# Kernel optimization log

Hardware: AMD Instinct MI355X
Metric: run time of the kernel (lower is better)

The kernel has to match this reference:

```python
import math
import jax, jax.numpy as jnp
import numpy as np
from jax import lax

# ---- static config (mirrors RPN init + typical torchvision anchor setup) ----
IMG_H = IMG_W = 800
LEVELS = [(200, 200, 4, 32), (100, 100, 8, 64), (50, 50, 16, 128), (25, 25, 32, 256), (13, 13, 64, 512)]  # (h, w, stride, anchor_size)
RATIOS = (0.5, 1.0, 2.0)
COUNTS = tuple(h * w * len(RATIOS) for (h, w, _, _) in LEVELS)  # (120000,30000,7500,1875,507)
A_TOTAL = sum(COUNTS)  # 159882
PRE_NMS = 2000
POST_NMS = 1000
NMS_THRESH = 0.7
MIN_SIZE = 1e-3
BBOX_CLIP = math.log(1000.0 / 16)


def make_anchors():
    parts = []
    for (h, w, stride, size) in LEVELS:
        ws = np.array([size * np.sqrt(1.0 / r) for r in RATIOS], np.float32)  # [3]
        hs = np.array([size * np.sqrt(r) for r in RATIOS], np.float32)
        sx = (np.arange(w, dtype=np.float32) + 0.5) * stride
        sy = (np.arange(h, dtype=np.float32) + 0.5) * stride
        cy, cx = np.meshgrid(sy, sx, indexing='ij')
        cx = cx.reshape(-1, 1)
        cy = cy.reshape(-1, 1)
        a = np.stack([cx - ws / 2, cy - hs / 2, cx + ws / 2, cy + hs / 2], axis=-1)  # [HW,3,4]
        parts.append(a.reshape(-1, 4))
    return np.concatenate(parts, 0).astype(np.float32)


def setup_inputs() -> dict:
    key = jax.random.key(0)
    k1, k2 = jax.random.split(key)
    scores = jax.random.normal(k1, (1, A_TOTAL), dtype=jnp.float32)
    deltas = jax.random.normal(k2, (A_TOTAL, 4), dtype=jnp.float32) * 0.5
    anchors = jnp.asarray(make_anchors())
    return {'scores': scores, 'deltas': deltas, 'anchors': anchors}


def _pairwise_iou(b):
    area = (b[:, 2] - b[:, 0]) * (b[:, 3] - b[:, 1])  # [K]
    lt = jnp.maximum(b[:, None, :2], b[None, :, :2])   # [K,K,2]
    rb = jnp.minimum(b[:, None, 2:], b[None, :, 2:])
    wh = jnp.maximum(rb - lt, 0.0)
    inter = wh[..., 0] * wh[..., 1]
    return inter / (area[:, None] + area[None, :] - inter)


def reference(scores, deltas, anchors):
    s_all = lax.stop_gradient(scores[0])  # original does cls.detach()
    # ---- box decode (torchvision-style) ----
    w = anchors[:, 2] - anchors[:, 0]
    h = anchors[:, 3] - anchors[:, 1]
    cx = anchors[:, 0] + 0.5 * w
    cy = anchors[:, 1] + 0.5 * h
    dx, dy = deltas[:, 0], deltas[:, 1]
    dw = jnp.minimum(deltas[:, 2], BBOX_CLIP)
    dh = jnp.minimum(deltas[:, 3], BBOX_CLIP)
    px = cx + dx * w
    py = cy + dy * h
    pw = jnp.exp(dw) * w
    ph = jnp.exp(dh) * h
    boxes = jnp.stack([px - 0.5 * pw, py - 0.5 * ph, px + 0.5 * pw, py + 0.5 * ph], axis=1)  # [A,4]
    # ---- per-level top-k over objectness ----
    idx_parts = []
    off = 0
    for c in COUNTS:
        k = min(PRE_NMS, c)
        _, ti = lax.top_k(lax.dynamic_slice_in_dim(s_all, off, c), k)
        idx_parts.append(ti + off)
        off += c
    top_idx = jnp.concatenate(idx_parts)  # [K=8382]
    K = top_idx.shape[0]
    s = s_all[top_idx]
    b = boxes[top_idx]
    # ---- clip to image + min-size validity (masked instead of compacted) ----
    b = jnp.stack([jnp.clip(b[:, 0], 0.0, IMG_W), jnp.clip(b[:, 1], 0.0, IMG_H),
                   jnp.clip(b[:, 2], 0.0, IMG_W), jnp.clip(b[:, 3], 0.0, IMG_H)], axis=1)
    valid = ((b[:, 2] - b[:, 0]) >= MIN_SIZE) & ((b[:, 3] - b[:, 1]) >= MIN_SIZE)
    # ---- per-level NMS offset; replicates original feature_mask[keep] indexing
    # (positional indexing into the full anchor-order level-id vector) ----
    fmask_full = np.concatenate([np.full(c, i, np.float32) for i, c in enumerate(COUNTS)])
    fmask = jnp.asarray(fmask_full[:K])
    box_max = jnp.max(jnp.where(valid[:, None], b, -jnp.inf))
    bn = b + (fmask * (box_max + 1.0))[:, None]
    # ---- greedy NMS on score-sorted candidates ----
    s_m = jnp.where(valid, s, -jnp.inf)
    order = jnp.argsort(-s_m)
    s_srt = s_m[order]
    b_srt = b[order]
    iou = _pairwise_iou(bn[order])  # [K,K] ~281MB
    ar = jnp.arange(K)

    def body(i, keep):
        sup = (iou[i] > NMS_THRESH) & (ar > i)
        return jnp.where(keep[i], keep & ~sup, keep)

    keep = lax.fori_loop(0, K, body, s_srt > -jnp.inf)
    final = jnp.where(keep, s_srt, -jnp.inf)
    out_s, oidx = lax.top_k(final, POST_NMS)  # top post_nms kept, score order; -inf pads
    out_b = b_srt[oidx]
    return out_b, out_s
```

## Files before the change

kernel.cpp:

```cpp
#include <hip/hip_runtime.h>
#include <math.h>

typedef unsigned int u32;
typedef unsigned long long u64;
typedef unsigned char u8;

#define K_TOT 8382
#define NCH 131
#define SC 4
#define NSC ((NCH + SC - 1) / SC)
#define CAP 1024
#define GCAP 32768
#define IMGSZ 800.0f

__device__ __constant__ int LOFF[5] = {0, 120000, 150000, 157500, 159375};
__device__ __constant__ int LCNT[5] = {120000, 30000, 7500, 1875, 507};
__device__ __constant__ int KSEL[5] = {2000, 2000, 2000, 1875, 507};
__device__ __constant__ int SELB[5] = {0, 2000, 4000, 6000, 7875};
__device__ __constant__ int HBS[4] = {0, 118, 148, 156};
__device__ __constant__ int GBS[6] = {0, 118, 148, 156, 158, 159};

static __device__ __forceinline__ u32 fkey(float x) {
    u32 u = __float_as_uint(x);
    u32 m = (u32)(((int)u) >> 31) | 0x80000000u;
    return u ^ m;
}

static __device__ __forceinline__ int lvl_of(int s) {
    return (s < 2000) ? 0 : (s < 4000) ? 1 : (s < 6000) ? 2 : (s < 7875) ? 3 : 4;
}

static __device__ __forceinline__ u32 rdl32(u32 v, int j) {
    return (u32)__builtin_amdgcn_readlane((int)v, j);
}
static __device__ __forceinline__ u64 rdlane64(u64 v, int j) {
    u32 lo = (u32)__builtin_amdgcn_readlane((int)(u32)v, j);
    u32 hi = (u32)__builtin_amdgcn_readlane((int)(u32)(v >> 32), j);
    return ((u64)hi << 32) | (u64)lo;
}

static __device__ __forceinline__ u32 wor32(u32 x) {
    x |= (u32)__builtin_amdgcn_update_dpp(0, (int)x, 0x111, 0xf, 0xf, true);
    x |= (u32)__builtin_amdgcn_update_dpp(0, (int)x, 0x112, 0xf, 0xf, true);
    x |= (u32)__builtin_amdgcn_update_dpp(0, (int)x, 0x114, 0xf, 0xf, true);
    x |= (u32)__builtin_amdgcn_update_dpp(0, (int)x, 0x118, 0xf, 0xf, true);
    x |= (u32)__builtin_amdgcn_update_dpp(0, (int)x, 0x142, 0xa, 0xf, true);
    x |= (u32)__builtin_amdgcn_update_dpp(0, (int)x, 0x143, 0xc, 0xf, true);
    return x;
}

static __device__ __forceinline__ void thresh_scan(const u32* hist, u32* scanbuf, int m,
                                                   u32 need, u32* sv, int t) {
    for (int i = t; i < m; i += 1024) scanbuf[i] = hist[m - 1 - i];
    __syncthreads();
    for (int ofs = 1; ofs < m; ofs <<= 1) {
        int i0 = t, i1 = t + 1024;
        u32 a0 = 0, a1 = 0;
        if (i0 < m && i0 >= ofs) a0 = scanbuf[i0 - ofs];
        if (i1 < m && i1 >= ofs) a1 = scanbuf[i1 - ofs];
        __syncthreads();
        if (i0 < m && i0 >= ofs) scanbuf[i0] += a0;
        if (i1 < m && i1 >= ofs) scanbuf[i1] += a1;
        __syncthreads();
    }
    for (int i = t; i < m; i += 1024) {
        u32 inc = scanbuf[i];
        u32 exc = i ? scanbuf[i - 1] : 0;
        if (inc >= need && exc < need) { sv[0] = (u32)(m - 1 - i); sv[1] = need - exc; }
    }
    __syncthreads();
}

__global__ __launch_bounds__(1024) void k_hist(const float* __restrict__ scores,
                                               u32* __restrict__ hist3) {
    __shared__ u32 lh[2048];
    int t = threadIdx.x;
    lh[t] = 0; lh[t + 1024] = 0;
    __syncthreads();
    int b = blockIdx.x;
    int l = (b < HBS[1]) ? 0 : (b < HBS[2]) ? 1 : 2;
    int i = (b - HBS[l]) * 1024 + t;
    if (i < LCNT[l]) atomicAdd(&lh[fkey(scores[LOFF[l] + i]) >> 21], 1u);
    __syncthreads();
    u32* h = hist3 + l * 2048;
    if (lh[t]) atomicAdd(&h[t], lh[t]);
    if (lh[t + 1024]) atomicAdd(&h[t + 1024], lh[t + 1024]);
}

__global__ __launch_bounds__(1024) void k_thresh(const u32* __restrict__ hist3,
                                                 u32* __restrict__ tinfo) {
    __shared__ u32 scanbuf[2048];
    __shared__ u32 sv[2];
    int l = blockIdx.x;
    int t = threadIdx.x;
    thresh_scan(hist3 + l * 2048, scanbuf, 2048, (u32)KSEL[l], sv, t);
    if (t == 0) { tinfo[l * 2] = sv[0]; tinfo[l * 2 + 1] = sv[1]; }
}

__global__ __launch_bounds__(1024) void k_gather(const float* __restrict__ scores,
                                                 const u32* __restrict__ tinfo,
                                                 u32* __restrict__ sel, u32* __restrict__ cgt,
                                                 u32* __restrict__ gcnt, u32* __restrict__ gidx,
                                                 u32* __restrict__ gkey) {
    int b = blockIdx.x;
    int l = (b < GBS[1]) ? 0 : (b < GBS[2]) ? 1 : (b < GBS[3]) ? 2 : (b < GBS[4]) ? 3 : 4;
    int i = (b - GBS[l]) * 1024 + threadIdx.x;
    if (i >= LCNT[l]) return;
    int off = LOFF[l], sb = SELB[l];
    if (l >= 3) { sel[sb + i] = (u32)(off + i); return; }
    u32 ky = fkey(scores[off + i]);
    u32 b1 = tinfo[l * 2];
    u32 top = ky >> 21;
    if (top > b1) {
        u32 p = atomicAdd(&cgt[l], 1u);
        sel[sb + p] = (u32)(off + i);
    } else if (top == b1) {
        u32 e = atomicAdd(&gcnt[l], 1u);
        if (e < GCAP) { gidx[l * GCAP + e] = (u32)i; gkey[l * GCAP + e] = ky; }
    }
}

__global__ __launch_bounds__(1024) void k_final(const u32* __restrict__ gidx,
                                                const u32* __restrict__ gkey,
                                                const u32* __restrict__ gcnt,
                                                const u32* __restrict__ tinfo,
                                                u32* __restrict__ sel) {
    __shared__ u32 hist[2048];
    __shared__ u32 scanbuf[2048];
    __shared__ u32 eqbuf[1024];
    __shared__ u32 sv[2];
    __shared__ u32 c2, ceq;
    int l = blockIdx.x;
    int t = threadIdx.x;
    int k = KSEL[l], sb = SELB[l], off = LOFF[l];
    u32 m = gcnt[l]; if (m > GCAP) m = GCAP;
    u32 b1 = tinfo[l * 2];
    u32 need = tinfo[l * 2 + 1];
    const u32* kb = gkey + l * GCAP;
    const u32* ib = gidx + l * GCAP;
    hist[t] = 0; hist[t + 1024] = 0; __syncthreads();
    for (u32 e = t; e < m; e += 1024) atomicAdd(&hist[(kb[e] >> 10) & 2047u], 1u);
    __syncthreads();
    thresh_scan(hist, scanbuf, 2048, need, sv, t);
    u32 b2 = sv[0], need2 = sv[1];
    __syncthreads();
    hist[t] = 0; __syncthreads();
    for (u32 e = t; e < m; e += 1024) {
        u32 ky = kb[e];
        if (((ky >> 10) & 2047u) == b2) atomicAdd(&hist[ky & 1023u], 1u);
    }
    __syncthreads();
    thresh_scan(hist, scanbuf, 1024, need2, sv, t);
    u32 T = (b1 << 21) | (b2 << 10) | sv[0];
    u32 take = sv[1];
    if (t == 0) { c2 = 0; ceq = 0; }
    __syncthreads();
    u32 nGTbin = need - take;
    u32 base2 = (u32)sb + (u32)k - need;
    for (u32 e = t; e < m; e += 1024) {
        u32 ky = kb[e];
        if (ky > T) { u32 p = atomicAdd(&c2, 1u); sel[base2 + p] = (u32)off + ib[e]; }
        else if (ky == T) { u32 q = atomicAdd(&ceq, 1u); if (q < 1024) eqbuf[q] = ib[e]; }
    }
    __syncthreads();
    if (t == 0) {
        int n = (ceq > 1024u) ? 1024 : (int)ceq;
        for (int a = 1; a < n; ++a) {
            u32 v = eqbuf[a]; int bq = a - 1;
            while (bq >= 0 && eqbuf[bq] > v) { eqbuf[bq + 1] = eqbuf[bq]; --bq; }
            eqbuf[bq + 1] = v;
        }
        for (u32 q = 0; q < take; ++q) sel[base2 + nGTbin + q] = (u32)off + eqbuf[q];
    }
}

__global__ void k_decode(const float* __restrict__ scores, const float4* __restrict__ deltas,
                         const float4* __restrict__ anchors, const u32* __restrict__ sel,
                         float4* __restrict__ candB, float* __restrict__ candS,
                         u32* __restrict__ candV, u32* __restrict__ candA) {
    int s = blockIdx.x * 256 + threadIdx.x;
    if (s >= K_TOT) return;
    u32 a = sel[s];
    float4 an = anchors[a];
    float4 dl = deltas[a];
    float sc = scores[a];
    float w = __fsub_rn(an.z, an.x), h = __fsub_rn(an.w, an.y);
    float cx = __fadd_rn(an.x, __fmul_rn(0.5f, w));
    float cy = __fadd_rn(an.y, __fmul_rn(0.5f, h));
    const float CLIPV = (float)4.1351665567423563;
    float dw = fminf(dl.z, CLIPV);
    float dh = fminf(dl.w, CLIPV);
    float px = __fadd_rn(cx, __fmul_rn(dl.x, w));
    float py = __fadd_rn(cy, __fmul_rn(dl.y, h));
    float pw = __fmul_rn((float)exp((double)dw), w);
    float ph = __fmul_rn((float)exp((double)dh), h);
    float x1 = __fsub_rn(px, __fmul_rn(0.5f, pw));
    float y1 = __fsub_rn(py, __fmul_rn(0.5f, ph));
    float x2 = __fadd_rn(px, __fmul_rn(0.5f, pw));
    float y2 = __fadd_rn(py, __fmul_rn(0.5f, ph));
    x1 = fminf(fmaxf(x1, 0.0f), IMGSZ);
    y1 = fminf(fmaxf(y1, 0.0f), IMGSZ);
    x2 = fminf(fmaxf(x2, 0.0f), IMGSZ);
    y2 = fminf(fmaxf(y2, 0.0f), IMGSZ);
    bool valid = (__fsub_rn(x2, x1) >= 0.001f) && (__fsub_rn(y2, y1) >= 0.001f);
    candB[s] = make_float4(x1, y1, x2, y2);
    candS[s] = sc;
    candV[s] = valid ? 1u : 0u;
    candA[s] = a;
}

__global__ __launch_bounds__(256) void k_rank_lvl(const float* __restrict__ candS,
                                                  const u32* __restrict__ candA,
                                                  u32* __restrict__ Praw) {
    __shared__ u64 tile[256];
    int l = blockIdx.z;
    int cnt = KSEL[l], base = SELB[l];
    int tx = blockIdx.x * 256;
    int ty = blockIdx.y * 256;
    if (tx >= cnt || ty >= cnt) return;
    int t = threadIdx.x;
    u64 Aj = ~0ull;
    if (tx + t < cnt) {
        int j = base + tx + t;
        Aj = ((u64)(~fkey(candS[j])) << 32) | (u64)candA[j];
    }
    tile[t] = Aj;
    __syncthreads();
    int si = ty + t;
    if (si >= cnt) return;
    int s = base + si;
    u64 A = ((u64)(~fkey(candS[s])) << 32) | (u64)candA[s];
    int r = 0;
#pragma unroll 8
    for (int q = 0; q < 256; ++q) r += (tile[q] < A);
    if (r) atomicAdd(&Praw[s], (u32)r);
}

__global__ __launch_bounds__(256) void k_rank_glob(const float* __restrict__ candS,
                                                   const u32* __restrict__ candV,
                                                   const u32* __restrict__ Praw,
                                                   u32* __restrict__ rank) {
    __shared__ u64 colB[256];
    int t = threadIdx.x;
    int cj = blockIdx.x * 256 + t;
    u64 B = ~0ull;
    if (cj < K_TOT) {
        u32 smk = candV[cj] ? fkey(candS[cj]) : 0x007FFFFFu;
        u32 Pj = (u32)SELB[lvl_of(cj)] + Praw[cj];
        B = ((u64)(~smk) << 32) | (u64)Pj;
    }
    colB[t] = B;
    __syncthreads();
    int s = blockIdx.y * 256 + t;
    if (s >= K_TOT) return;
    u32 smk = candV[s] ? fkey(candS[s]) : 0x007FFFFFu;
    u32 Ps = (u32)SELB[lvl_of(s)] + Praw[s];
    u64 myB = ((u64)(~smk) << 32) | (u64)Ps;
    int cnt = 0;
#pragma unroll 8
    for (int j = 0; j < 256; ++j) cnt += (colB[j] < myB);
    if (cnt) atomicAdd(&rank[s], (u32)cnt);
}

__global__ void k_scatter(const float4* __restrict__ candB, const float* __restrict__ candS,
                          const u32* __restrict__ candV, const u32* __restrict__ rank,
                          float4* __restrict__ sB, float* __restrict__ sArea,
                          float* __restrict__ sS, u32* __restrict__ sV) {
    int s = blockIdx.x * 256 + threadIdx.x;
    if (s >= K_TOT) return;
    u32 r = rank[s];
    float4 b = candB[s];
    float area = __fmul_rn(__fsub_rn(b.z, b.x), __fsub_rn(b.w, b.y));
    sB[r] = b; sArea[r] = area; sS[r] = candS[s]; sV[r] = candV[s];
}

__global__ __launch_bounds__(256) void k_mask(const float4* __restrict__ sB,
                                              const float* __restrict__ sArea,
                                              const u32* __restrict__ sV,
                                              u64* __restrict__ vwords,
                                              u64* __restrict__ diag, u32* __restrict__ ecnt,
                                              ulonglong2* __restrict__ epack,
                                              u64* __restrict__ dmask) {
    __shared__ float4 cb[64];
    __shared__ float ca[64];
    int wd = blockIdx.x;
    int t = threadIdx.x;
    if (t < 64) {
        int j = wd * 64 + t;
        if (j < K_TOT) { cb[t] = sB[j]; ca[t] = sArea[j]; }
        else { cb[t] = make_float4(0.f, 0.f, 0.f, 0.f); ca[t] = 0.f; }
    }
    __syncthreads();
    int i = blockIdx.y * 256 + t;
    if (i >= K_TOT) return;
    int dwr = i >> 6;
    if (wd < dwr) return;
    float4 bi = sB[i];
    float ai = sArea[i];
    u64 bits = 0;
    int jbase = wd * 64;
    for (int j2 = 0; j2 < 64; ++j2) {
        int j = jbase + j2;
        if (j > i && j < K_TOT) {
            float4 bj = cb[j2];
            float ltx = fmaxf(bi.x, bj.x), lty = fmaxf(bi.y, bj.y);
            float rbx = fminf(bi.z, bj.z), rby = fminf(bi.w, bj.w);
            float wx = fmaxf(__fsub_rn(rbx, ltx), 0.0f);
            float wy = fmaxf(__fsub_rn(rby, lty), 0.0f);
            float inter = __fmul_rn(wx, wy);
            if (inter > 0.0f) {
                float uni = __fsub_rn(__fadd_rn(ai, ca[j2]), inter);
                float iou = inter / uni;
                if (iou > 0.7f) bits |= (1ull << j2);
            }
        }
    }
    if (wd == dwr) {
        diag[i] = bits;
        u64 vb = __ballot(sV[i] != 0u);
        u64 db = __ballot(bits != 0ull);
        if ((i & 63) == 0) { vwords[wd] = vb; dmask[wd] = db; }
    } else if (bits != 0ull) {
        u32 p = atomicAdd(&ecnt[wd], 1u);
        if (p < CAP) epack[wd * CAP + p] = make_ulonglong2((u64)i, bits);
    }
}

__global__ __launch_bounds__(512) void k_scan(const u64* __restrict__ diag,
                                              const u64* __restrict__ vwords,
                                              const u32* __restrict__ ecnt,
                                              const ulonglong2* __restrict__ tpack,
                                              const u64* __restrict__ dmask,
                                              const float4* __restrict__ sB,
                                              const float* __restrict__ sS,
                                              float* __restrict__ out) {
    __shared__ u64 sKeepArr[NSC * SC];
    __shared__ u32 pc[NCH + 1];
    __shared__ u32 sProg;
    int t = threadIdx.x;
    int w = t >> 6, lane = t & 63;
    if (t == 0) sProg = 0;
    if (t < NSC * SC) sKeepArr[t] = 0;
    __syncthreads();
    if (w < 4) {
        for (int C = w; C < NSC; C += 4) {
            int w0 = C * SC;
            int t0 = w0, t1 = w0 + 1, t2 = w0 + 2, t3 = w0 + 3;
            bool x1v = t1 < NCH, x2v = t2 < NCH, x3v = t3 < NCH;
            int q1 = x1v ? t1 : 0, q2 = x2v ? t2 : 0, q3 = x3v ? t3 : 0;
            u32 c0 = ecnt[t0], c1 = x1v ? ecnt[q1] : 0, c2 = x2v ? ecnt[q2] : 0, c3 = x3v ? ecnt[q3] : 0;
            if (c0 > CAP) c0 = CAP;
            if (c1 > CAP) c1 = CAP;
            if (c2 > CAP) c2 = CAP;
            if (c3 > CAP) c3 = CAP;
            u64 vw0 = vwords[t0];
            u64 vw1 = x1v ? vwords[q1] : 0;
            u64 vw2 = x2v ? vwords[q2] : 0;
            u64 vw3 = x3v ? vwords[q3] : 0;
            u64 dmw0 = dmask[t0];
            u64 dmw1 = x1v ? dmask[q1] : 0;
            u64 dmw2 = x2v ? dmask[q2] : 0;
            u64 dmw3 = x3v ? dmask[q3] : 0;
            u64 D0 = diag[t0 * 64 + lane];
            u64 D1 = diag[q1 * 64 + lane];
            u64 D2 = diag[q2 * 64 + lane];
            u64 D3 = diag[q3 * 64 + lane];
            ulonglong2 E00 = tpack[(size_t)t0 * CAP + lane];
            ulonglong2 E01 = tpack[(size_t)t0 * CAP + 64 + lane];
            ulonglong2 E10 = tpack[(size_t)q1 * CAP + lane];
            ulonglong2 E11 = tpack[(size_t)q1 * CAP + 64 + lane];
            ulonglong2 E20 = tpack[(size_t)q2 * CAP + lane];
            ulonglong2 E21 = tpack[(size_t)q2 * CAP + 64 + lane];
            ulonglong2 E30 = tpack[(size_t)q3 * CAP + lane];
            ulonglong2 E31 = tpack[(size_t)q3 * CAP + 64 + lane];
            u32 s00 = (u32)E00.x, s01 = (u32)E01.x, s10 = (u32)E10.x, s11 = (u32)E11.x;
            u32 s20 = (u32)E20.x, s21 = (u32)E21.x, s30 = (u32)E30.x, s31 = (u32)E31.x;
            u32 h00 = s00 >> 6, h01 = s01 >> 6, h10 = s10 >> 6, h11 = s11 >> 6;
            u32 h20 = s20 >> 6, h21 = s21 >> 6, h30 = s30 >> 6, h31 = s31 >> 6;
            if (C > 0) {
                for (;;) {
                    u32 p = __hip_atomic_load(&sProg, __ATOMIC_ACQUIRE, __HIP_MEMORY_SCOPE_WORKGROUP);
                    if (p >= (u32)C) break;
                    if ((u32)C > p + 1u) __builtin_amdgcn_s_sleep(2);
                }
            }
            u64 K00 = sKeepArr[h00 < (u32)NCH ? h00 : 0u];
            u64 K01 = sKeepArr[h01 < (u32)NCH ? h01 : 0u];
            u64 K10 = sKeepArr[h10 < (u32)NCH ? h10 : 0u];
            u64 K11 = sKeepArr[h11 < (u32)NCH ? h11 : 0u];
            u64 K20 = sKeepArr[h20 < (u32)NCH ? h20 : 0u];
            u64 K21 = sKeepArr[h21 < (u32)NCH ? h21 : 0u];
            u64 K30 = sKeepArr[h30 < (u32)NCH ? h30 : 0u];
            u64 K31 = sKeepArr[h31 < (u32)NCH ? h31 : 0u];
            u64 m = 0;
            if ((u32)lane < c0 && ((K00 >> (s00 & 63u)) & 1ull)) m = E00.y;
            if ((u32)(lane + 64) < c0 && ((K01 >> (s01 & 63u)) & 1ull)) m |= E01.y;
            if (c0 > 128u) {
                for (u32 e = 128u + (u32)lane; e < c0; e += 64u) {
                    ulonglong2 Et = tpack[(size_t)t0 * CAP + e];
                    u32 si = (u32)Et.x;
                    if ((sKeepArr[si >> 6] >> (si & 63u)) & 1ull) m |= Et.y;
                }
            }
            u32 lo = wor32((u32)m), hi = wor32((u32)(m >> 32));
            u64 inc = ((u64)rdl32(hi, 63) << 32) | (u64)rdl32(lo, 63);
            u64 alive0 = vw0 & ~inc;
            if (dmw0) {
                u64 d = dmw0 & alive0;
                while (d) {
                    int j = __builtin_ctzll(d);
                    d &= d - 1;
                    if ((alive0 >> j) & 1ull) { alive0 &= ~rdlane64(D0, j); d &= alive0; }
                }
            }
            u64 kwA = (h10 == (u32)t0) ? alive0 : K10;
            u64 kwB = (h11 == (u32)t0) ? alive0 : K11;
            m = 0;
            if ((u32)lane < c1 && ((kwA >> (s10 & 63u)) & 1ull)) m = E10.y;
            if ((u32)(lane + 64) < c1 && ((kwB >> (s11 & 63u)) & 1ull)) m |= E11.y;
            if (c1 > 128u) {
                for (u32 e = 128u + (u32)lane; e < c1; e += 64u) {
                    ulonglong2 Et = tpack[(size_t)q1 * CAP + e];
                    u32 si = (u32)Et.x; u32 hh = si >> 6;
                    u64 kw = (hh == (u32)t0) ? alive0 : sKeepArr[hh];
                    if ((kw >> (si & 63u)) & 1ull) m |= Et.y;
                }
            }
            lo = wor32((u32)m); hi = wor32((u32)(m >> 32));
            inc = ((u64)rdl32(hi, 63) << 32) | (u64)rdl32(lo, 63);
            u64 alive1 = vw1 & ~inc;
            if (dmw1) {
                u64 d = dmw1 & alive1;
                while (d) {
                    int j = __builtin_ctzll(d);
                    d &= d - 1;
                    if ((alive1 >> j) & 1ull) { alive1 &= ~rdlane64(D1, j); d &= alive1; }
                }
            }
            kwA = (h20 == (u32)t0) ? alive0 : (h20 == (u32)t1) ? alive1 : K20;
            kwB = (h21 == (u32)t0) ? alive0 : (h21 == (u32)t1) ? alive1 : K21;
            m = 0;
            if ((u32)lane < c2 && ((kwA >> (s20 & 63u)) & 1ull)) m = E20.y;
            if ((u32)(lane + 64) < c2 && ((kwB >> (s21 & 63u)) & 1ull)) m |= E21.y;
            if (c2 > 128u) {
                for (u32 e = 128u + (u32)lane; e < c2; e += 64u) {
                    ulonglong2 Et = tpack[(size_t)q2 * CAP + e];
                    u32 si = (u32)Et.x; u32 hh = si >> 6;
                    u64 kw = (hh == (u32)t0) ? alive0 : (hh == (u32)t1) ? alive1 : sKeepArr[hh];
                    if ((kw >> (si & 63u)) & 1ull) m |= Et.y;
                }
            }
            lo = wor32((u32)m); hi = wor32((u32)(m >> 32));
            inc = ((u64)rdl32(hi, 63) << 32) | (u64)rdl32(lo, 63);
            u64 alive2 = vw2 & ~inc;
            if (dmw2) {
                u64 d = dmw2 & alive2;
                while (d) {
                    int j = __builtin_ctzll(d);
                    d &= d - 1;
                    if ((alive2 >> j) & 1ull) { alive2 &= ~rdlane64(D2, j); d &= alive2; }
                }
            }
            kwA = (h30 == (u32)t0) ? alive0 : (h30 == (u32)t1) ? alive1 : (h30 == (u32)t2) ? alive2 : K30;
            kwB = (h31 == (u32)t0) ? alive0 : (h31 == (u32)t1) ? alive1 : (h31 == (u32)t2) ? alive2 : K31;
            m = 0;
            if ((u32)lane < c3 && ((kwA >> (s30 & 63u)) & 1ull)) m = E30.y;
            if ((u32)(lane + 64) < c3 && ((kwB >> (s31 & 63u)) & 1ull)) m |= E31.y;
            if (c3 > 128u) {
                for (u32 e = 128u + (u32)lane; e < c3; e += 64u) {
                    ulonglong2 Et = tpack[(size_t)q3 * CAP + e];
                    u32 si = (u32)Et.x; u32 hh = si >> 6;
                    u64 kw = (hh == (u32)t0) ? alive0 : (hh == (u32)t1) ? alive1
                           : (hh == (u32)t2) ? alive2 : sKeepArr[hh];
                    if ((kw >> (si & 63u)) & 1ull) m |= Et.y;
                }
            }
            lo = wor32((u32)m); hi = wor32((u32)(m >> 32));
            inc = ((u64)rdl32(hi, 63) << 32) | (u64)rdl32(lo, 63);
            u64 alive3 = vw3 & ~inc;
            if (dmw3) {
                u64 d = dmw3 & alive3;
                while (d) {
                    int j = __builtin_ctzll(d);
                    d &= d - 1;
                    if ((alive3 >> j) & 1ull) { alive3 &= ~rdlane64(D3, j); d &= alive3; }
                }
            }
            if (lane == 0) {
                sKeepArr[t0] = alive0;
                sKeepArr[t1] = alive1;
                sKeepArr[t2] = alive2;
                sKeepArr[t3] = alive3;
                __hip_atomic_store(&sProg, (u32)(C + 1), __ATOMIC_RELEASE, __HIP_MEMORY_SCOPE_WORKGROUP);
            }
        }
    }
    __syncthreads();
    if (t < NCH) pc[t + 1] = (u32)__popcll(sKeepArr[t]);
    if (t == 0) pc[0] = 0;
    __syncthreads();
    for (int ofs = 1; ofs < NCH; ofs <<= 1) {
        int i = t + 1;
        u32 v = 0;
        bool p = (t < NCH) && (i - ofs >= 1);
        if (p) v = pc[i - ofs];
        __syncthreads();
        if (p) pc[i] += v;
        __syncthreads();
    }
    u32 nk = pc[NCH];
    for (int i = t; i < K_TOT; i += 512) {
        int wi = i >> 6, b = i & 63;
        u64 kw = sKeepArr[wi];
        u32 kb = pc[wi] + (u32)__popcll(kw & ((1ull << b) - 1ull));
        bool kp = (kw >> b) & 1ull;
        if (kp) {
            if (kb < 1000u) {
                float4 bx = sB[i];
                out[kb * 4 + 0] = bx.x; out[kb * 4 + 1] = bx.y;
                out[kb * 4 + 2] = bx.z; out[kb * 4 + 3] = bx.w;
                out[4000 + kb] = sS[i];
            }
        } else {
            u32 q = (u32)i - kb;
            u32 slot = nk + q;
            if (slot < 1000u) {
                float4 bx = sB[i];
                out[slot * 4 + 0] = bx.x; out[slot * 4 + 1] = bx.y;
                out[slot * 4 + 2] = bx.z; out[slot * 4 + 3] = bx.w;
                out[4000 + slot] = -INFINITY;
            }
        }
    }
}

static constexpr size_t al256(size_t x) { return (x + 255) & ~(size_t)255; }
static constexpr size_t KB4 = (size_t)K_TOT * 4;
static constexpr size_t KB16 = (size_t)K_TOT * 16;
static constexpr size_t O_RANK = 0;
static constexpr size_t O_PRAW = al256(O_RANK + KB4);
static constexpr size_t O_ECNT = al256(O_PRAW + KB4);
static constexpr size_t O_HIST = al256(O_ECNT + (size_t)NCH * 4);
static constexpr size_t O_CGT = al256(O_HIST + (size_t)3 * 2048 * 4);
static constexpr size_t O_GCNT = al256(O_CGT + 3 * 4);
static constexpr size_t MEMSET_BYTES = al256(O_GCNT + 3 * 4);
static constexpr size_t O_TINFO = MEMSET_BYTES;
static constexpr size_t O_SEL = al256(O_TINFO + 6 * 4);
static constexpr size_t O_GIDX = al256(O_SEL + KB4);
static constexpr size_t O_GKEY = al256(O_GIDX + (size_t)3 * GCAP * 4);
static constexpr size_t O_CANDB = al256(O_GKEY + (size_t)3 * GCAP * 4);
static constexpr size_t O_CANDS = al256(O_CANDB + KB16);
static constexpr size_t O_CANDV = al256(O_CANDS + KB4);
static constexpr size_t O_CANDA = al256(O_CANDV + KB4);
static constexpr size_t O_SB = al256(O_CANDA + KB4);
static constexpr size_t O_SAREA = al256(O_SB + KB16);
static constexpr size_t O_SS = al256(O_SAREA + KB4);
static constexpr size_t O_SV = al256(O_SS + KB4);
static constexpr size_t O_VW = al256(O_SV + KB4);
static constexpr size_t O_DMASK = al256(O_VW + (size_t)NCH * 8);
static constexpr size_t O_DIAG = al256(O_DMASK + (size_t)NCH * 8);
static constexpr size_t O_EPACK = al256(O_DIAG + (size_t)(NCH * 64) * 8);

extern "C" void kernel_launch(void* const* d_in, const int* in_sizes, int n_in,
                              void* d_out, int out_size, void* d_ws, size_t ws_size,
                              hipStream_t stream) {
    const float* scores = (const float*)d_in[0];
    const float4* deltas = (const float4*)d_in[1];
    const float4* anchors = (const float4*)d_in[2];
    float* out = (float*)d_out;
    char* ws = (char*)d_ws;

    u32* rank = (u32*)(ws + O_RANK);
    u32* Praw = (u32*)(ws + O_PRAW);
    u32* ecnt = (u32*)(ws + O_ECNT);
    u32* hist3 = (u32*)(ws + O_HIST);
    u32* cgt = (u32*)(ws + O_CGT);
    u32* gcnt = (u32*)(ws + O_GCNT);
    u32* tinfo = (u32*)(ws + O_TINFO);
    u32* sel = (u32*)(ws + O_SEL);
    u32* gidx = (u32*)(ws + O_GIDX);
    u32* gkey = (u32*)(ws + O_GKEY);
    float4* candB = (float4*)(ws + O_CANDB);
    float* candS = (float*)(ws + O_CANDS);
    u32* candV = (u32*)(ws + O_CANDV);
    u32* candA = (u32*)(ws + O_CANDA);
    float4* sB = (float4*)(ws + O_SB);
    float* sArea = (float*)(ws + O_SAREA);
    float* sS = (float*)(ws + O_SS);
    u32* sV = (u32*)(ws + O_SV);
    u64* vwords = (u64*)(ws + O_VW);
    u64* dmask = (u64*)(ws + O_DMASK);
    u64* diag = (u64*)(ws + O_DIAG);
    ulonglong2* epack = (ulonglong2*)(ws + O_EPACK);

    hipMemsetAsync(ws, 0, MEMSET_BYTES, stream);

    const int NBLK = (K_TOT + 255) / 256;
    k_hist<<<156, 1024, 0, stream>>>(scores, hist3);
    k_thresh<<<3, 1024, 0, stream>>>(hist3, tinfo);
    k_gather<<<159, 1024, 0, stream>>>(scores, tinfo, sel, cgt, gcnt, gidx, gkey);
    k_final<<<3, 1024, 0, stream>>>(gidx, gkey, gcnt, tinfo, sel);
    k_decode<<<NBLK, 256, 0, stream>>>(scores, deltas, anchors, sel, candB, candS, candV, candA);
    k_rank_lvl<<<dim3(8, 8, 5), 256, 0, stream>>>(candS, candA, Praw);
    k_rank_glob<<<dim3(NBLK, NBLK), 256, 0, stream>>>(candS, candV, Praw, rank);
    k_scatter<<<NBLK, 256, 0, stream>>>(candB, candS, candV, rank, sB, sArea, sS, sV);
    k_mask<<<dim3(NCH, NBLK), 256, 0, stream>>>(sB, sArea, sV, vwords, diag, ecnt, epack, dmask);
    k_scan<<<1, 512, 0, stream>>>(diag, vwords, ecnt, epack, dmask, sB, sS, out);
}
```

Baseline: 194.6 us.

## Fuse threshold scan into histogram via last-block pattern and decode into final select

```diff
diff --git a/kernel.cpp b/kernel.cpp
--- a/kernel.cpp
+++ b/kernel.cpp
@@ -49,137 +49,53 @@
     return x;
 }
 
-static __device__ __forceinline__ void thresh_scan(const u32* hist, u32* scanbuf, int m,
-                                                   u32 need, u32* sv, int t) {
-    for (int i = t; i < m; i += 1024) scanbuf[i] = hist[m - 1 - i];
-    __syncthreads();
-    for (int ofs = 1; ofs < m; ofs <<= 1) {
-        int i0 = t, i1 = t + 1024;
-        u32 a0 = 0, a1 = 0;
-        if (i0 < m && i0 >= ofs) a0 = scanbuf[i0 - ofs];
-        if (i1 < m && i1 >= ofs) a1 = scanbuf[i1 - ofs];
-        __syncthreads();
-        if (i0 < m && i0 >= ofs) scanbuf[i0] += a0;
-        if (i1 < m && i1 >= ofs) scanbuf[i1] += a1;
-        __syncthreads();
-    }
-    for (int i = t; i < m; i += 1024) {
-        u32 inc = scanbuf[i];
-        u32 exc = i ? scanbuf[i - 1] : 0;
-        if (inc >= need && exc < need) { sv[0] = (u32)(m - 1 - i); sv[1] = need - exc; }
-    }
-    __syncthreads();
-}
-
-__global__ __launch_bounds__(1024) void k_hist(const float* __restrict__ scores,
-                                               u32* __restrict__ hist3) {
-    __shared__ u32 lh[2048];
-    int t = threadIdx.x;
-    lh[t] = 0; lh[t + 1024] = 0;
-    __syncthreads();
-    int b = blockIdx.x;
-    int l = (b < HBS[1]) ? 0 : (b < HBS[2]) ? 1 : 2;
-    int i = (b - HBS[l]) * 1024 + t;
-    if (i < LCNT[l]) atomicAdd(&lh[fkey(scores[LOFF[l] + i]) >> 21], 1u);
-    __syncthreads();
-    u32* h = hist3 + l * 2048;
-    if (lh[t]) atomicAdd(&h[t], lh[t]);
-    if (lh[t + 1024]) atomicAdd(&h[t + 1024], lh[t + 1024]);
-}
-
-__global__ __launch_bounds__(1024) void k_thresh(const u32* __restrict__ hist3,
-                                                 u32* __restrict__ tinfo) {
-    __shared__ u32 scanbuf[2048];
-    __shared__ u32 sv[2];
-    int l = blockIdx.x;
-    int t = threadIdx.x;
-    thresh_scan(hist3 + l * 2048, scanbuf, 2048, (u32)KSEL[l], sv, t);
-    if (t == 0) { tinfo[l * 2] = sv[0]; tinfo[l * 2 + 1] = sv[1]; }
-}
-
-__global__ __launch_bounds__(1024) void k_gather(const float* __restrict__ scores,
-                                                 const u32* __restrict__ tinfo,
-                                                 u32* __restrict__ sel, u32* __restrict__ cgt,
-                                                 u32* __restrict__ gcnt, u32* __restrict__ gidx,
-                                                 u32* __restrict__ gkey) {
-    int b = blockIdx.x;
-    int l = (b < GBS[1]) ? 0 : (b < GBS[2]) ? 1 : (b < GBS[3]) ? 2 : (b < GBS[4]) ? 3 : 4;
-    int i = (b - GBS[l]) * 1024 + threadIdx.x;
-    if (i >= LCNT[l]) return;
-    int off = LOFF[l], sb = SELB[l];
-    if (l >= 3) { sel[sb + i] = (u32)(off + i); return; }
-    u32 ky = fkey(scores[off + i]);
-    u32 b1 = tinfo[l * 2];
-    u32 top = ky >> 21;
-    if (top > b1) {
-        u32 p = atomicAdd(&cgt[l], 1u);
-        sel[sb + p] = (u32)(off + i);
-    } else if (top == b1) {
-        u32 e = atomicAdd(&gcnt[l], 1u);
-        if (e < GCAP) { gidx[l * GCAP + e] = (u32)i; gkey[l * GCAP + e] = ky; }
-    }
-}
-
-__global__ __launch_bounds__(1024) void k_final(const u32* __restrict__ gidx,
-                                                const u32* __restrict__ gkey,
-                                                const u32* __restrict__ gcnt,
-                                                const u32* __restrict__ tinfo,
-                                                u32* __restrict__ sel) {
-    __shared__ u32 hist[2048];
-    __shared__ u32 scanbuf[2048];
-    __shared__ u32 eqbuf[1024];
-    __shared__ u32 sv[2];
-    __shared__ u32 c2, ceq;
-    int l = blockIdx.x;
-    int t = threadIdx.x;
-    int k = KSEL[l], sb = SELB[l], off = LOFF[l];
-    u32 m = gcnt[l]; if (m > GCAP) m = GCAP;
-    u32 b1 = tinfo[l * 2];
-    u32 need = tinfo[l * 2 + 1];
-    const u32* kb = gkey + l * GCAP;
-    const u32* ib = gidx + l * GCAP;
-    hist[t] = 0; hist[t + 1024] = 0; __syncthreads();
-    for (u32 e = t; e < m; e += 1024) atomicAdd(&hist[(kb[e] >> 10) & 2047u], 1u);
-    __syncthreads();
-    thresh_scan(hist, scanbuf, 2048, need, sv, t);
-    u32 b2 = sv[0], need2 = sv[1];
-    __syncthreads();
-    hist[t] = 0; __syncthreads();
-    for (u32 e = t; e < m; e += 1024) {
-        u32 ky = kb[e];
-        if (((ky >> 10) & 2047u) == b2) atomicAdd(&hist[ky & 1023u], 1u);
-    }
-    __syncthreads();
-    thresh_scan(hist, scanbuf, 1024, need2, sv, t);
-    u32 T = (b1 << 21) | (b2 << 10) | sv[0];
-    u32 take = sv[1];
-    if (t == 0) { c2 = 0; ceq = 0; }
-    __syncthreads();
-    u32 nGTbin = need - take;
-    u32 base2 = (u32)sb + (u32)k - need;
-    for (u32 e = t; e < m; e += 1024) {
-        u32 ky = kb[e];
-        if (ky > T) { u32 p = atomicAdd(&c2, 1u); sel[base2 + p] = (u32)off + ib[e]; }
-        else if (ky == T) { u32 q = atomicAdd(&ceq, 1u); if (q < 1024) eqbuf[q] = ib[e]; }
-    }
-    __syncthreads();
-    if (t == 0) {
-        int n = (ceq > 1024u) ? 1024 : (int)ceq;
-        for (int a = 1; a < n; ++a) {
-            u32 v = eqbuf[a]; int bq = a - 1;
-            while (bq >= 0 && eqbuf[bq] > v) { eqbuf[bq + 1] = eqbuf[bq]; --bq; }
-            eqbuf[bq + 1] = v;
-        }
-        for (u32 q = 0; q < take; ++q) sel[base2 + nGTbin + q] = (u32)off + eqbuf[q];
-    }
-}
-
-__global__ void k_decode(const float* __restrict__ scores, const float4* __restrict__ deltas,
-                         const float4* __restrict__ anchors, const u32* __restrict__ sel,
-                         float4* __restrict__ candB, float* __restrict__ candS,
-                         u32* __restrict__ candV, u32* __restrict__ candA) {
-    int s = blockIdx.x * 256 + threadIdx.x;
-    if (s >= K_TOT) return;
+static __device__ __forceinline__ u32 wscan_inc(u32 x, int lane) {
+    for (int d = 1; d < 64; d <<= 1) {
+        u32 v = (u32)__shfl_up((int)x, d, 64);
+        if (lane >= d) x += v;
+    }
+    return x;
+}
+
+static __device__ __forceinline__ void thresh_scan2(const u32* hist, int m, u32 need,
+                                                    u32* sv, u32* wsum, int t) {
+    int lane = t & 63, wv = t >> 6;
+    u32 a, b = 0, s;
+    if (m == 2048) {
+        a = hist[2047 - 2 * t];
+        b = hist[2046 - 2 * t];
+        s = a + b;
+    } else {
+        a = hist[1023 - t];
+        s = a;
+    }
+    u32 winc = wscan_inc(s, lane);
+    if (lane == 63) wsum[wv] = winc;
+    __syncthreads();
+    u32 wexc = 0;
+#pragma unroll
+    for (int i = 0; i < 16; ++i) { u32 v = wsum[i]; if (i < wv) wexc += v; }
+    u32 exc = wexc + winc - s;
+    if (m == 2048) {
+        u32 inc0 = exc + a;
+        if (inc0 >= need && exc < need) { sv[0] = (u32)(2047 - 2 * t); sv[1] = need - exc; }
+        u32 inc1 = inc0 + b;
+        if (inc1 >= need && inc0 < need) { sv[0] = (u32)(2046 - 2 * t); sv[1] = need - inc0; }
+    } else {
+        u32 inc0 = exc + a;
+        if (inc0 >= need && exc < need) { sv[0] = (u32)(1023 - t); sv[1] = need - exc; }
+    }
+    __syncthreads();
+}
+
+static __device__ __forceinline__ void decode_one(int s, const float* __restrict__ scores,
+                                                  const float4* __restrict__ deltas,
+                                                  const float4* __restrict__ anchors,
+                                                  const u32* __restrict__ sel,
+                                                  float4* __restrict__ candB,
+                                                  float* __restrict__ candS,
+                                                  u32* __restrict__ candV,
+                                                  u32* __restrict__ candA) {
     u32 a = sel[s];
     float4 an = anchors[a];
     float4 dl = deltas[a];
@@ -207,6 +123,133 @@
     candS[s] = sc;
     candV[s] = valid ? 1u : 0u;
     candA[s] = a;
+}
+
+__global__ __launch_bounds__(1024) void k_hist(const float* __restrict__ scores,
+                                               u32* __restrict__ hist3,
+                                               u32* __restrict__ hdone,
+                                               u32* __restrict__ tinfo) {
+    __shared__ u32 lh[2048];
+    __shared__ u32 wsum[16];
+    __shared__ u32 sv[2];
+    __shared__ u32 slast;
+    int t = threadIdx.x;
+    lh[t] = 0; lh[t + 1024] = 0;
+    __syncthreads();
+    int b = blockIdx.x;
+    int l = (b < HBS[1]) ? 0 : (b < HBS[2]) ? 1 : 2;
+    int i = (b - HBS[l]) * 1024 + t;
+    if (i < LCNT[l]) atomicAdd(&lh[fkey(scores[LOFF[l] + i]) >> 21], 1u);
+    __syncthreads();
+    u32* h = hist3 + l * 2048;
+    if (lh[t]) atomicAdd(&h[t], lh[t]);
+    if (lh[t + 1024]) atomicAdd(&h[t + 1024], lh[t + 1024]);
+    __threadfence();
+    __syncthreads();
+    if (t == 0) slast = atomicAdd(hdone, 1u);
+    __syncthreads();
+    if (slast != 155u) return;
+    for (int lv = 0; lv < 3; ++lv) {
+        const u32* hg = hist3 + lv * 2048;
+        lh[t] = __hip_atomic_load(&hg[t], __ATOMIC_RELAXED, __HIP_MEMORY_SCOPE_AGENT);
+        lh[t + 1024] = __hip_atomic_load(&hg[t + 1024], __ATOMIC_RELAXED, __HIP_MEMORY_SCOPE_AGENT);
+        __syncthreads();
+        thresh_scan2(lh, 2048, (u32)KSEL[lv], sv, wsum, t);
+        if (t == 0) { tinfo[lv * 2] = sv[0]; tinfo[lv * 2 + 1] = sv[1]; }
+        __syncthreads();
+    }
+}
+
+__global__ __launch_bounds__(1024) void k_gather(const float* __restrict__ scores,
+                                                 const u32* __restrict__ tinfo,
+                                                 u32* __restrict__ sel, u32* __restrict__ cgt,
+                                                 u32* __restrict__ gcnt, u32* __restrict__ gidx,
+                                                 u32* __restrict__ gkey) {
+    int b = blockIdx.x;
+    int l = (b < GBS[1]) ? 0 : (b < GBS[2]) ? 1 : (b < GBS[3]) ? 2 : (b < GBS[4]) ? 3 : 4;
+    int i = (b - GBS[l]) * 1024 + threadIdx.x;
+    if (i >= LCNT[l]) return;
+    int off = LOFF[l], sb = SELB[l];
+    if (l >= 3) { sel[sb + i] = (u32)(off + i); return; }
+    u32 ky = fkey(scores[off + i]);
+    u32 b1 = tinfo[l * 2];
+    u32 top = ky >> 21;
+    if (top > b1) {
+        u32 p = atomicAdd(&cgt[l], 1u);
+        sel[sb + p] = (u32)(off + i);
+    } else if (top == b1) {
+        u32 e = atomicAdd(&gcnt[l], 1u);
+        if (e < GCAP) { gidx[l * GCAP + e] = (u32)i; gkey[l * GCAP + e] = ky; }
+    }
+}
+
+__global__ __launch_bounds__(1024) void k_final(const u32* __restrict__ gidx,
+                                                const u32* __restrict__ gkey,
+                                                const u32* __restrict__ gcnt,
+                                                const u32* __restrict__ tinfo,
+                                                u32* __restrict__ sel,
+                                                const float* __restrict__ scores,
+                                                const float4* __restrict__ deltas,
+                                                const float4* __restrict__ anchors,
+                                                float4* __restrict__ candB,
+                                                float* __restrict__ candS,
+                                                u32* __restrict__ candV,
+                                                u32* __restrict__ candA) {
+    __shared__ u32 hist[2048];
+    __shared__ u32 eqbuf[1024];
+    __shared__ u32 wsum[16];
+    __shared__ u32 sv[2];
+    __shared__ u32 c2, ceq;
+    int l = blockIdx.x;
+    int t = threadIdx.x;
+    int k = KSEL[l], sb = SELB[l], off = LOFF[l];
+    if (l >= 3) {
+        for (int s2 = sb + t; s2 < sb + k; s2 += 1024)
+            decode_one(s2, scores, deltas, anchors, sel, candB, candS, candV, candA);
+        return;
+    }
+    u32 m = gcnt[l]; if (m > GCAP) m = GCAP;
+    u32 b1 = tinfo[l * 2];
+    u32 need = tinfo[l * 2 + 1];
+    const u32* kb = gkey + l * GCAP;
+    const u32* ib = gidx + l * GCAP;
+    hist[t] = 0; hist[t + 1024] = 0; __syncthreads();
+    for (u32 e = t; e < m; e += 1024) atomicAdd(&hist[(kb[e] >> 10) & 2047u], 1u);
+    __syncthreads();
+    thresh_scan2(hist, 2048, need, sv, wsum, t);
+    u32 b2 = sv[0], need2 = sv[1];
+    __syncthreads();
+    hist[t] = 0; __syncthreads();
+    for (u32 e = t; e < m; e += 1024) {
+        u32 ky = kb[e];
+        if (((ky >> 10) & 2047u) == b2) atomicAdd(&hist[ky & 1023u], 1u);
+    }
+    __syncthreads();
+    thresh_scan2(hist, 1024, need2, sv, wsum, t);
+    u32 T = (b1 << 21) | (b2 << 10) | sv[0];
+    u32 take = sv[1];
+    if (t == 0) { c2 = 0; ceq = 0; }
+    __syncthreads();
+    u32 nGTbin = need - take;
+    u32 base2 = (u32)sb + (u32)k - need;
+    for (u32 e = t; e < m; e += 1024) {
+        u32 ky = kb[e];
+        if (ky > T) { u32 p = atomicAdd(&c2, 1u); sel[base2 + p] = (u32)off + ib[e]; }
+        else if (ky == T) { u32 q = atomicAdd(&ceq, 1u); if (q < 1024) eqbuf[q] = ib[e]; }
+    }
+    __syncthreads();
+    if (t == 0) {
+        int n = (ceq > 1024u) ? 1024 : (int)ceq;
+        for (int a = 1; a < n; ++a) {
+            u32 v = eqbuf[a]; int bq = a - 1;
+            while (bq >= 0 && eqbuf[bq] > v) { eqbuf[bq + 1] = eqbuf[bq]; --bq; }
+            eqbuf[bq + 1] = v;
+        }
+        for (u32 q = 0; q < take; ++q) sel[base2 + nGTbin + q] = (u32)off + eqbuf[q];
+    }
+    __syncthreads();
+    for (int s2 = sb + t; s2 < sb + k; s2 += 1024)
+        decode_one(s2, scores, deltas, anchors, sel, candB, candS, candV, candA);
 }
 
 __global__ __launch_bounds__(256) void k_rank_lvl(const float* __restrict__ candS,
@@ -543,7 +586,8 @@
 static constexpr size_t O_HIST = al256(O_ECNT + (size_t)NCH * 4);
 static constexpr size_t O_CGT = al256(O_HIST + (size_t)3 * 2048 * 4);
 static constexpr size_t O_GCNT = al256(O_CGT + 3 * 4);
-static constexpr size_t MEMSET_BYTES = al256(O_GCNT + 3 * 4);
+static constexpr size_t O_HDONE = al256(O_GCNT + 3 * 4);
+static constexpr size_t MEMSET_BYTES = al256(O_HDONE + 4);
 static constexpr size_t O_TINFO = MEMSET_BYTES;
 static constexpr size_t O_SEL = al256(O_TINFO + 6 * 4);
 static constexpr size_t O_GIDX = al256(O_SEL + KB4);
@@ -576,6 +620,7 @@
     u32* hist3 = (u32*)(ws + O_HIST);
     u32* cgt = (u32*)(ws + O_CGT);
     u32* gcnt = (u32*)(ws + O_GCNT);
+    u32* hdone = (u32*)(ws + O_HDONE);
     u32* tinfo = (u32*)(ws + O_TINFO);
     u32* sel = (u32*)(ws + O_SEL);
     u32* gidx = (u32*)(ws + O_GIDX);
@@ -596,11 +641,10 @@
     hipMemsetAsync(ws, 0, MEMSET_BYTES, stream);
 
     const int NBLK = (K_TOT + 255) / 256;
-    k_hist<<<156, 1024, 0, stream>>>(scores, hist3);
-    k_thresh<<<3, 1024, 0, stream>>>(hist3, tinfo);
+    k_hist<<<156, 1024, 0, stream>>>(scores, hist3, hdone, tinfo);
     k_gather<<<159, 1024, 0, stream>>>(scores, tinfo, sel, cgt, gcnt, gidx, gkey);
-    k_final<<<3, 1024, 0, stream>>>(gidx, gkey, gcnt, tinfo, sel);
-    k_decode<<<NBLK, 256, 0, stream>>>(scores, deltas, anchors, sel, candB, candS, candV, candA);
+    k_final<<<5, 1024, 0, stream>>>(gidx, gkey, gcnt, tinfo, sel,
+                                    scores, deltas, anchors, candB, candS, candV, candA);
     k_rank_lvl<<<dim3(8, 8, 5), 256, 0, stream>>>(candS, candA, Praw);
     k_rank_glob<<<dim3(NBLK, NBLK), 256, 0, stream>>>(candS, candV, Praw, rank);
     k_scatter<<<NBLK, 256, 0, stream>>>(candB, candS, candV, rank, sB, sArea, sS, sV);
```

Measured after the change: 234.1 us. 1.2x slower.
